# Performance work log

Measured on AMD Instinct MI355X. Metric: run time of the kernel, lower is better.

## Reference

```python
import jax, jax.numpy as jnp
import numpy as np


def sign_fn(x):
    # torch.sign(torch.sign(x) + 0.5): maps x >= 0 -> +1, x < 0 -> -1 (zero -> +1)
    return jnp.where(x >= 0, 1.0, -1.0).astype(x.dtype)


def setup_inputs() -> dict:
    key = jax.random.key(0)
    kx, kw, kb = jax.random.split(key, 3)
    TOKENS, IN, OUT = 8192, 4096, 4096
    x = jax.random.normal(kx, (TOKENS, IN), dtype=jnp.float32)
    weight = jax.random.normal(kw, (OUT, IN), dtype=jnp.float32)
    bias = jax.random.normal(kb, (OUT,), dtype=jnp.float32)
    return {"x": x, "weight": weight, "bias": bias}


def reference(x, weight, bias):
    b_weight = sign_fn(weight)  # [out, in], values in {+1, -1}
    b_bias = sign_fn(bias)      # [out]
    # nn.functional.linear: y = x @ W^T + b
    return jnp.einsum('ti,oi->to', x, b_weight) + b_bias
```

## Files before the change

### kernel.cpp

```cpp
#include <hip/hip_runtime.h>


typedef __attribute__((ext_vector_type(4))) int   i32x4;
typedef __attribute__((ext_vector_type(8))) short short8;
typedef __attribute__((ext_vector_type(4))) float f32x4;

constexpr int M = 8192;
constexpr int N = 4096;
constexpr int K = 4096;

constexpr int MT = 128;
constexpr int NT = 128;
constexpr int KT = 64;

__device__ __forceinline__ void load_lds16(const void* g, void* l) {
    __builtin_amdgcn_global_load_lds(
        (const __attribute__((address_space(1))) unsigned int*)g,
        (__attribute__((address_space(3))) unsigned int*)l, 16, 0, 0);
}

__global__ __launch_bounds__(256) void prep_x(
    const float* __restrict__ X, signed char* __restrict__ Xq,
    float* __restrict__ Scale) {
    const int row = blockIdx.x;
    const int t   = threadIdx.x;
    const float4* xr = reinterpret_cast<const float4*>(X + (size_t)row * K);

    float4 v[4];
    float mx = 0.f;
#pragma unroll
    for (int i = 0; i < 4; ++i) {
        v[i] = xr[t + i * 256];
        mx = fmaxf(mx, fmaxf(fmaxf(fabsf(v[i].x), fabsf(v[i].y)),
                             fmaxf(fabsf(v[i].z), fabsf(v[i].w))));
    }
#pragma unroll
    for (int off = 32; off > 0; off >>= 1)
        mx = fmaxf(mx, __shfl_down(mx, off));
    __shared__ float wmax[4];
    if ((t & 63) == 0) wmax[t >> 6] = mx;
    __syncthreads();
    float rmax = fmaxf(fmaxf(wmax[0], wmax[1]), fmaxf(wmax[2], wmax[3]));
    rmax = fmaxf(rmax, 1e-20f);
    const float inv = 127.f / rmax;
    if (t == 0) Scale[row] = rmax * (1.f / 127.f);

    unsigned int* out = reinterpret_cast<unsigned int*>(Xq + (size_t)row * K);
#pragma unroll
    for (int i = 0; i < 4; ++i) {
        int q0 = (int)rintf(v[i].x * inv);
        int q1 = (int)rintf(v[i].y * inv);
        int q2 = (int)rintf(v[i].z * inv);
        int q3 = (int)rintf(v[i].w * inv);
        unsigned int p = (q0 & 255) | ((q1 & 255) << 8) |
                         ((q2 & 255) << 16) | ((unsigned)(q3 & 255) << 24);
        out[t + i * 256] = p;
    }
}

__global__ __launch_bounds__(256) void prep_w(
    const float* __restrict__ W, signed char* __restrict__ Wq) {
    size_t i = (size_t)blockIdx.x * 256 + threadIdx.x;
    const float4* s = reinterpret_cast<const float4*>(W) + i * 2;
    float4 a = s[0], b = s[1];
    auto sg = [](float f) -> unsigned int { return (f >= 0.f) ? 1u : 0xFFu; };
    uint2 o;
    o.x = sg(a.x) | (sg(a.y) << 8) | (sg(a.z) << 16) | (sg(a.w) << 24);
    o.y = sg(b.x) | (sg(b.y) << 8) | (sg(b.z) << 16) | (sg(b.w) << 24);
    reinterpret_cast<uint2*>(Wq)[i] = o;
}

__global__ __launch_bounds__(256) void gemm_i8(
    const signed char* __restrict__ Aq, const signed char* __restrict__ Bq,
    const float* __restrict__ Scale, const float* __restrict__ Bias,
    float* __restrict__ OUT) {
    __shared__ signed char As[MT * KT];
    __shared__ signed char Bs[NT * KT];

    const int tid  = threadIdx.x;
    const int lane = tid & 63;
    const int wave = tid >> 6;
    const int wm   = wave >> 1;
    const int wn   = wave & 1;

    const int m0 = blockIdx.y * MT;
    const int n0 = blockIdx.x * NT;

    const int rl  = lane & 15;
    const int kq  = (lane >> 4) * 16;

    const int srow = wave * 32 + (lane >> 2);
    const int scol = (lane & 3) * 16;
    const signed char* gA = Aq + (size_t)(m0 + srow) * K + scol;
    const signed char* gB = Bq + (size_t)(n0 + srow) * K + scol;
    signed char* lA0 = &As[(wave * 32) * KT];
    signed char* lA1 = &As[(wave * 32 + 16) * KT];
    signed char* lB0 = &Bs[(wave * 32) * KT];
    signed char* lB1 = &Bs[(wave * 32 + 16) * KT];

    i32x4 acc[4][4];
#pragma unroll
    for (int mi = 0; mi < 4; ++mi)
#pragma unroll
        for (int ni = 0; ni < 4; ++ni)
            acc[mi][ni] = (i32x4){0, 0, 0, 0};

    for (int k0 = 0; k0 < K; k0 += KT) {
        load_lds16(gA + k0, lA0);
        load_lds16(gA + k0 + 16 * K, lA1);
        load_lds16(gB + k0, lB0);
        load_lds16(gB + k0 + 16 * K, lB1);
        __syncthreads();

        i32x4 a[4], b[4];
#pragma unroll
        for (int mi = 0; mi < 4; ++mi)
            a[mi] = *reinterpret_cast<const i32x4*>(&As[(wm * 64 + mi * 16 + rl) * KT + kq]);
#pragma unroll
        for (int ni = 0; ni < 4; ++ni)
            b[ni] = *reinterpret_cast<const i32x4*>(&Bs[(wn * 64 + ni * 16 + rl) * KT + kq]);
#pragma unroll
        for (int mi = 0; mi < 4; ++mi)
#pragma unroll
            for (int ni = 0; ni < 4; ++ni)
                acc[mi][ni] = __builtin_amdgcn_mfma_i32_16x16x64_i8(
                    a[mi], b[ni], acc[mi][ni], 0, 0, 0);
        __syncthreads();
    }

#pragma unroll
    for (int ni = 0; ni < 4; ++ni) {
        int gcol = n0 + wn * 64 + ni * 16 + rl;
        float sb = (Bias[gcol] >= 0.f) ? 1.f : -1.f;
#pragma unroll
        for (int mi = 0; mi < 4; ++mi) {
            int growb = m0 + wm * 64 + mi * 16 + (lane >> 4) * 4;
            float4 sc = *reinterpret_cast<const float4*>(&Scale[growb]);
            OUT[(size_t)(growb + 0) * N + gcol] = (float)acc[mi][ni][0] * sc.x + sb;
            OUT[(size_t)(growb + 1) * N + gcol] = (float)acc[mi][ni][1] * sc.y + sb;
            OUT[(size_t)(growb + 2) * N + gcol] = (float)acc[mi][ni][2] * sc.z + sb;
            OUT[(size_t)(growb + 3) * N + gcol] = (float)acc[mi][ni][3] * sc.w + sb;
        }
    }
}

constexpr int LDSS = 40;
constexpr int KTB  = 32;
__device__ __forceinline__ unsigned short f2b(float f) {
    unsigned int u = __builtin_bit_cast(unsigned int, f);
    u += 0x7FFFu + ((u >> 16) & 1u);
    return (unsigned short)(u >> 16);
}
__global__ __launch_bounds__(256) void binlin_fallback(
    const float* __restrict__ X, const float* __restrict__ W,
    const float* __restrict__ B, float* __restrict__ OUT) {
    __shared__ unsigned short As[MT][LDSS];
    __shared__ unsigned short Bs[NT][LDSS];
    const int tid  = threadIdx.x;
    const int lane = tid & 63;
    const int wave = tid >> 6;
    const int wm   = wave >> 1;
    const int wn   = wave & 1;
    const int m0 = blockIdx.y * MT;
    const int n0 = blockIdx.x * NT;
    const int rl = lane & 15;
    const int kq = (lane >> 4) * 8;
    f32x4 acc[4][4];
#pragma unroll
    for (int mi = 0; mi < 4; ++mi)
#pragma unroll
        for (int ni = 0; ni < 4; ++ni)
            acc[mi][ni] = (f32x4){0.f, 0.f, 0.f, 0.f};
    for (int k0 = 0; k0 < K; k0 += KTB) {
#pragma unroll
        for (int it = 0; it < 4; ++it) {
            int g = tid + it * 256, row = g >> 3, c4 = (g & 7) << 2;
            float4 v = *reinterpret_cast<const float4*>(&X[(size_t)(m0 + row) * K + k0 + c4]);
            ushort4 h;
            h.x = f2b(v.x); h.y = f2b(v.y); h.z = f2b(v.z); h.w = f2b(v.w);
            *reinterpret_cast<ushort4*>(&As[row][c4]) = h;
        }
#pragma unroll
        for (int it = 0; it < 4; ++it) {
            int g = tid + it * 256, row = g >> 3, c4 = (g & 7) << 2;
            float4 v = *reinterpret_cast<const float4*>(&W[(size_t)(n0 + row) * K + k0 + c4]);
            ushort4 h;
            h.x = (v.x >= 0.f) ? 0x3F80u : 0xBF80u;
            h.y = (v.y >= 0.f) ? 0x3F80u : 0xBF80u;
            h.z = (v.z >= 0.f) ? 0x3F80u : 0xBF80u;
            h.w = (v.w >= 0.f) ? 0x3F80u : 0xBF80u;
            *reinterpret_cast<ushort4*>(&Bs[row][c4]) = h;
        }
        __syncthreads();
        short8 a[4], b[4];
#pragma unroll
        for (int mi = 0; mi < 4; ++mi)
            a[mi] = *reinterpret_cast<const short8*>(&As[wm * 64 + mi * 16 + rl][kq]);
#pragma unroll
        for (int ni = 0; ni < 4; ++ni)
            b[ni] = *reinterpret_cast<const short8*>(&Bs[wn * 64 + ni * 16 + rl][kq]);
#pragma unroll
        for (int mi = 0; mi < 4; ++mi)
#pragma unroll
            for (int ni = 0; ni < 4; ++ni)
                acc[mi][ni] = __builtin_amdgcn_mfma_f32_16x16x32_bf16(
                    a[mi], b[ni], acc[mi][ni], 0, 0, 0);
        __syncthreads();
    }
#pragma unroll
    for (int ni = 0; ni < 4; ++ni) {
        int gcol = n0 + wn * 64 + ni * 16 + rl;
        float sb = (B[gcol] >= 0.f) ? 1.f : -1.f;
#pragma unroll
        for (int mi = 0; mi < 4; ++mi) {
            int growb = m0 + wm * 64 + mi * 16 + (lane >> 4) * 4;
#pragma unroll
            for (int r = 0; r < 4; ++r)
                OUT[(size_t)(growb + r) * N + gcol] = acc[mi][ni][r] + sb;
        }
    }
}

extern "C" void kernel_launch(void* const* d_in, const int* in_sizes, int n_in,
                              void* d_out, int out_size, void* d_ws, size_t ws_size,
                              hipStream_t stream) {
    const float* x  = (const float*)d_in[0];
    const float* w  = (const float*)d_in[1];
    const float* b  = (const float*)d_in[2];
    float* out      = (float*)d_out;

    const size_t need = (size_t)M * K + (size_t)N * K + (size_t)M * sizeof(float);
    if (ws_size >= need) {
        signed char* Xq = (signed char*)d_ws;
        signed char* Wq = Xq + (size_t)M * K;
        float* Scale    = (float*)(Wq + (size_t)N * K);

        prep_x<<<dim3(M), dim3(256), 0, stream>>>(x, Xq, Scale);
        prep_w<<<dim3((unsigned)((size_t)N * K / 8 / 256)), dim3(256), 0, stream>>>(w, Wq);
        dim3 grid(N / NT, M / MT);
        gemm_i8<<<grid, dim3(256), 0, stream>>>(Xq, Wq, Scale, b, out);
    } else {
        dim3 grid(N / NT, M / MT);
        binlin_fallback<<<grid, dim3(256), 0, stream>>>(x, w, b, out);
    }
}
```

Baseline: 433.6 us.

## Rewrite int8 GEMM with 256x256 tiles, 4-deep LDS ring, swizzle, and fused prep

Fuses the two prep kernels into one launch. The int8 GEMM is rebuilt around 256x256 block tiles with 8 waves, a 4-stage global-to-LDS ring buffer that keeps three loads in flight, XOR-swizzled LDS columns against bank conflicts, grouped block ordering for L2 reuse, and s_setprio around the MFMA burst. The aim is to hide global-load latency and raise arithmetic intensity, which the single-buffered 128x128 version could not do. The costs are a much larger LDS footprint (128 KB per block) and more registers, which limit occupancy.

```diff
diff --git a/kernel.cpp b/kernel.cpp
--- a/kernel.cpp
+++ b/kernel.cpp
@@ -9,9 +9,12 @@
 constexpr int N = 4096;
 constexpr int K = 4096;
 
-constexpr int MT = 128;
-constexpr int NT = 128;
-constexpr int KT = 64;
+constexpr int BM = 256, BN = 256, BK = 64;
+constexpr int NTILES = K / BK;
+constexpr int TILE_A = BM * BK;
+constexpr int TILE_B = BN * BK;
+constexpr int BUFSZ  = TILE_A + TILE_B;
+constexpr int RING   = 4;
 
 __device__ __forceinline__ void load_lds16(const void* g, void* l) {
     __builtin_amdgcn_global_load_lds(
@@ -19,123 +22,152 @@
         (__attribute__((address_space(3))) unsigned int*)l, 16, 0, 0);
 }
 
-__global__ __launch_bounds__(256) void prep_x(
-    const float* __restrict__ X, signed char* __restrict__ Xq,
+__global__ __launch_bounds__(256) void prep_fused(
+    const float* __restrict__ X, const float* __restrict__ W,
+    signed char* __restrict__ Xq, signed char* __restrict__ Wq,
     float* __restrict__ Scale) {
-    const int row = blockIdx.x;
-    const int t   = threadIdx.x;
-    const float4* xr = reinterpret_cast<const float4*>(X + (size_t)row * K);
-
-    float4 v[4];
-    float mx = 0.f;
-#pragma unroll
-    for (int i = 0; i < 4; ++i) {
-        v[i] = xr[t + i * 256];
-        mx = fmaxf(mx, fmaxf(fmaxf(fabsf(v[i].x), fabsf(v[i].y)),
-                             fmaxf(fabsf(v[i].z), fabsf(v[i].w))));
-    }
-#pragma unroll
-    for (int off = 32; off > 0; off >>= 1)
-        mx = fmaxf(mx, __shfl_down(mx, off));
     __shared__ float wmax[4];
-    if ((t & 63) == 0) wmax[t >> 6] = mx;
-    __syncthreads();
-    float rmax = fmaxf(fmaxf(wmax[0], wmax[1]), fmaxf(wmax[2], wmax[3]));
-    rmax = fmaxf(rmax, 1e-20f);
-    const float inv = 127.f / rmax;
-    if (t == 0) Scale[row] = rmax * (1.f / 127.f);
-
-    unsigned int* out = reinterpret_cast<unsigned int*>(Xq + (size_t)row * K);
-#pragma unroll
-    for (int i = 0; i < 4; ++i) {
-        int q0 = (int)rintf(v[i].x * inv);
-        int q1 = (int)rintf(v[i].y * inv);
-        int q2 = (int)rintf(v[i].z * inv);
-        int q3 = (int)rintf(v[i].w * inv);
-        unsigned int p = (q0 & 255) | ((q1 & 255) << 8) |
-                         ((q2 & 255) << 16) | ((unsigned)(q3 & 255) << 24);
-        out[t + i * 256] = p;
-    }
-}
-
-__global__ __launch_bounds__(256) void prep_w(
-    const float* __restrict__ W, signed char* __restrict__ Wq) {
-    size_t i = (size_t)blockIdx.x * 256 + threadIdx.x;
-    const float4* s = reinterpret_cast<const float4*>(W) + i * 2;
-    float4 a = s[0], b = s[1];
-    auto sg = [](float f) -> unsigned int { return (f >= 0.f) ? 1u : 0xFFu; };
-    uint2 o;
-    o.x = sg(a.x) | (sg(a.y) << 8) | (sg(a.z) << 16) | (sg(a.w) << 24);
-    o.y = sg(b.x) | (sg(b.y) << 8) | (sg(b.z) << 16) | (sg(b.w) << 24);
-    reinterpret_cast<uint2*>(Wq)[i] = o;
-}
-
-__global__ __launch_bounds__(256) void gemm_i8(
+    const int t = threadIdx.x;
+
+    if (blockIdx.x < M) {
+        const int row = blockIdx.x;
+        const float4* xr = reinterpret_cast<const float4*>(X + (size_t)row * K);
+        float4 v[4];
+        float mx = 0.f;
+#pragma unroll
+        for (int i = 0; i < 4; ++i) {
+            v[i] = xr[t + i * 256];
+            mx = fmaxf(mx, fmaxf(fmaxf(fabsf(v[i].x), fabsf(v[i].y)),
+                                 fmaxf(fabsf(v[i].z), fabsf(v[i].w))));
+        }
+#pragma unroll
+        for (int off = 32; off > 0; off >>= 1)
+            mx = fmaxf(mx, __shfl_down(mx, off));
+        if ((t & 63) == 0) wmax[t >> 6] = mx;
+        __syncthreads();
+        float rmax = fmaxf(fmaxf(wmax[0], wmax[1]), fmaxf(wmax[2], wmax[3]));
+        rmax = fmaxf(rmax, 1e-20f);
+        const float inv = 127.f / rmax;
+        if (t == 0) Scale[row] = rmax * (1.f / 127.f);
+
+        unsigned int* out = reinterpret_cast<unsigned int*>(Xq + (size_t)row * K);
+#pragma unroll
+        for (int i = 0; i < 4; ++i) {
+            int q0 = (int)rintf(v[i].x * inv);
+            int q1 = (int)rintf(v[i].y * inv);
+            int q2 = (int)rintf(v[i].z * inv);
+            int q3 = (int)rintf(v[i].w * inv);
+            unsigned int p = (q0 & 255) | ((q1 & 255) << 8) |
+                             ((q2 & 255) << 16) | ((unsigned)(q3 & 255) << 24);
+            out[t + i * 256] = p;
+        }
+    } else {
+        size_t i = (size_t)(blockIdx.x - M) * 256 + t;
+        const float4* s = reinterpret_cast<const float4*>(W) + i * 2;
+        float4 a = s[0], b = s[1];
+        auto sg = [](float f) -> unsigned int { return (f >= 0.f) ? 1u : 0xFFu; };
+        uint2 o;
+        o.x = sg(a.x) | (sg(a.y) << 8) | (sg(a.z) << 16) | (sg(a.w) << 24);
+        o.y = sg(b.x) | (sg(b.y) << 8) | (sg(b.z) << 16) | (sg(b.w) << 24);
+        reinterpret_cast<uint2*>(Wq)[i] = o;
+    }
+}
+
+template <int VMN>
+__device__ __forceinline__ void kstep(const signed char* smem, int t,
+                                      int wm, int wn, int rl, int cq16,
+                                      i32x4 (&acc)[8][4]) {
+    asm volatile("s_waitcnt vmcnt(%0)" :: "i"(VMN) : "memory");
+    __builtin_amdgcn_s_barrier();
+    asm volatile("" ::: "memory");
+
+    const signed char* Ab = smem + (t & (RING - 1)) * BUFSZ;
+    const signed char* Bb = Ab + TILE_A;
+    i32x4 a[8], b[4];
+#pragma unroll
+    for (int mi = 0; mi < 8; ++mi)
+        a[mi] = *reinterpret_cast<const i32x4*>(
+            Ab + (wm * 128 + mi * 16 + rl) * BK + cq16);
+#pragma unroll
+    for (int ni = 0; ni < 4; ++ni)
+        b[ni] = *reinterpret_cast<const i32x4*>(
+            Bb + (wn * 64 + ni * 16 + rl) * BK + cq16);
+
+    __builtin_amdgcn_s_setprio(1);
+#pragma unroll
+    for (int mi = 0; mi < 8; ++mi)
+#pragma unroll
+        for (int ni = 0; ni < 4; ++ni)
+            acc[mi][ni] = __builtin_amdgcn_mfma_i32_16x16x64_i8(
+                a[mi], b[ni], acc[mi][ni], 0, 0, 0);
+    __builtin_amdgcn_s_setprio(0);
+
+    asm volatile("" ::: "memory");
+    __builtin_amdgcn_s_barrier();
+}
+
+__global__ __launch_bounds__(512, 2) void gemm_i8_p(
     const signed char* __restrict__ Aq, const signed char* __restrict__ Bq,
     const float* __restrict__ Scale, const float* __restrict__ Bias,
     float* __restrict__ OUT) {
-    __shared__ signed char As[MT * KT];
-    __shared__ signed char Bs[NT * KT];
+    __shared__ signed char smem[RING * BUFSZ];
 
     const int tid  = threadIdx.x;
     const int lane = tid & 63;
-    const int wave = tid >> 6;
-    const int wm   = wave >> 1;
-    const int wn   = wave & 1;
-
-    const int m0 = blockIdx.y * MT;
-    const int n0 = blockIdx.x * NT;
-
-    const int rl  = lane & 15;
-    const int kq  = (lane >> 4) * 16;
-
-    const int srow = wave * 32 + (lane >> 2);
-    const int scol = (lane & 3) * 16;
-    const signed char* gA = Aq + (size_t)(m0 + srow) * K + scol;
-    const signed char* gB = Bq + (size_t)(n0 + srow) * K + scol;
-    signed char* lA0 = &As[(wave * 32) * KT];
-    signed char* lA1 = &As[(wave * 32 + 16) * KT];
-    signed char* lB0 = &Bs[(wave * 32) * KT];
-    signed char* lB1 = &Bs[(wave * 32 + 16) * KT];
-
-    i32x4 acc[4][4];
-#pragma unroll
-    for (int mi = 0; mi < 4; ++mi)
+    const int w    = tid >> 6;
+    const int wm   = w >> 2;
+    const int wn   = w & 3;
+    const int rl   = lane & 15;
+    const int cq16 = (((lane >> 4) ^ ((rl >> 1) & 3)) << 4);
+
+    const int wg  = blockIdx.x;
+    const int lin = (wg & 7) * 64 + (wg >> 3);
+    const int n0  = (lin & 15) * BN;
+    const int m0  = (lin >> 4) * BM;
+
+    const int srow = tid >> 2;
+    const int cg   = ((tid & 3) ^ ((srow >> 1) & 3)) * 16;
+    const signed char* gA0 = Aq + (size_t)(m0 + srow)       * K + cg;
+    const signed char* gA1 = Aq + (size_t)(m0 + 128 + srow) * K + cg;
+    const signed char* gB0 = Bq + (size_t)(n0 + srow)       * K + cg;
+    const signed char* gB1 = Bq + (size_t)(n0 + 128 + srow) * K + cg;
+    signed char* lbase = smem + w * 1024;
+
+    auto stage = [&](int t) {
+        signed char* d = lbase + (t & (RING - 1)) * BUFSZ;
+        const size_t ko = (size_t)t * BK;
+        load_lds16(gA0 + ko, d);
+        load_lds16(gA1 + ko, d + 8192);
+        load_lds16(gB0 + ko, d + TILE_A);
+        load_lds16(gB1 + ko, d + TILE_A + 8192);
+    };
+
+    i32x4 acc[8][4];
+#pragma unroll
+    for (int mi = 0; mi < 8; ++mi)
 #pragma unroll
         for (int ni = 0; ni < 4; ++ni)
             acc[mi][ni] = (i32x4){0, 0, 0, 0};
 
-    for (int k0 = 0; k0 < K; k0 += KT) {
-        load_lds16(gA + k0, lA0);
-        load_lds16(gA + k0 + 16 * K, lA1);
-        load_lds16(gB + k0, lB0);
-        load_lds16(gB + k0 + 16 * K, lB1);
-        __syncthreads();
-
-        i32x4 a[4], b[4];
-#pragma unroll
-        for (int mi = 0; mi < 4; ++mi)
-            a[mi] = *reinterpret_cast<const i32x4*>(&As[(wm * 64 + mi * 16 + rl) * KT + kq]);
-#pragma unroll
-        for (int ni = 0; ni < 4; ++ni)
-            b[ni] = *reinterpret_cast<const i32x4*>(&Bs[(wn * 64 + ni * 16 + rl) * KT + kq]);
-#pragma unroll
-        for (int mi = 0; mi < 4; ++mi)
-#pragma unroll
-            for (int ni = 0; ni < 4; ++ni)
-                acc[mi][ni] = __builtin_amdgcn_mfma_i32_16x16x64_i8(
-                    a[mi], b[ni], acc[mi][ni], 0, 0, 0);
-        __syncthreads();
-    }
+    stage(0); stage(1); stage(2);
+
+    int t = 0;
+    for (; t < NTILES - 3; ++t) {
+        stage(t + 3);
+        kstep<12>(smem, t, wm, wn, rl, cq16, acc);
+    }
+    kstep<8>(smem, t, wm, wn, rl, cq16, acc); ++t;
+    kstep<4>(smem, t, wm, wn, rl, cq16, acc); ++t;
+    kstep<0>(smem, t, wm, wn, rl, cq16, acc);
 
 #pragma unroll
     for (int ni = 0; ni < 4; ++ni) {
-        int gcol = n0 + wn * 64 + ni * 16 + rl;
-        float sb = (Bias[gcol] >= 0.f) ? 1.f : -1.f;
-#pragma unroll
-        for (int mi = 0; mi < 4; ++mi) {
-            int growb = m0 + wm * 64 + mi * 16 + (lane >> 4) * 4;
-            float4 sc = *reinterpret_cast<const float4*>(&Scale[growb]);
+        const int gcol = n0 + wn * 64 + ni * 16 + rl;
+        const float sb = (Bias[gcol] >= 0.f) ? 1.f : -1.f;
+#pragma unroll
+        for (int mi = 0; mi < 8; ++mi) {
+            const int growb = m0 + wm * 128 + mi * 16 + (lane >> 4) * 4;
+            const float4 sc = *reinterpret_cast<const float4*>(&Scale[growb]);
             OUT[(size_t)(growb + 0) * N + gcol] = (float)acc[mi][ni][0] * sc.x + sb;
             OUT[(size_t)(growb + 1) * N + gcol] = (float)acc[mi][ni][1] * sc.y + sb;
             OUT[(size_t)(growb + 2) * N + gcol] = (float)acc[mi][ni][2] * sc.z + sb;
@@ -144,6 +176,8 @@
     }
 }
 
+constexpr int MT   = 128;
+constexpr int NTF  = 128;
 constexpr int LDSS = 40;
 constexpr int KTB  = 32;
 __device__ __forceinline__ unsigned short f2b(float f) {
@@ -155,14 +189,14 @@
     const float* __restrict__ X, const float* __restrict__ W,
     const float* __restrict__ B, float* __restrict__ OUT) {
     __shared__ unsigned short As[MT][LDSS];
-    __shared__ unsigned short Bs[NT][LDSS];
+    __shared__ unsigned short Bs[NTF][LDSS];
     const int tid  = threadIdx.x;
     const int lane = tid & 63;
     const int wave = tid >> 6;
     const int wm   = wave >> 1;
     const int wn   = wave & 1;
     const int m0 = blockIdx.y * MT;
-    const int n0 = blockIdx.x * NT;
+    const int n0 = blockIdx.x * NTF;
     const int rl = lane & 15;
     const int kq = (lane >> 4) * 8;
     f32x4 acc[4][4];
@@ -235,12 +269,13 @@
         signed char* Wq = Xq + (size_t)M * K;
         float* Scale    = (float*)(Wq + (size_t)N * K);
 
-        prep_x<<<dim3(M), dim3(256), 0, stream>>>(x, Xq, Scale);
-        prep_w<<<dim3((unsigned)((size_t)N * K / 8 / 256)), dim3(256), 0, stream>>>(w, Wq);
-        dim3 grid(N / NT, M / MT);
-        gemm_i8<<<grid, dim3(256), 0, stream>>>(Xq, Wq, Scale, b, out);
+        const unsigned prepw_blocks = (unsigned)((size_t)N * K / 8 / 256);
+        prep_fused<<<dim3(M + prepw_blocks), dim3(256), 0, stream>>>(x, w, Xq, Wq, Scale);
+
+        gemm_i8_p<<<dim3((M / BM) * (N / BN)), dim3(512), 0, stream>>>(
+            Xq, Wq, Scale, b, out);
     } else {
-        dim3 grid(N / NT, M / MT);
+        dim3 grid(N / NTF, M / MT);
         binlin_fallback<<<grid, dim3(256), 0, stream>>>(x, w, b, out);
     }
 }
```

After: 404.6 us. 6.7% less time.
